# Performance work log

Hardware: AMD Instinct MI355X
Metric: run time of the kernel (lower is better)

The kernel has to match this reference:

```python
import jax, jax.numpy as jnp
import numpy as np

EPS = 1e-08


def conv(x, w, b, stride):
    y = jax.lax.conv_general_dilated(x, w, (stride, stride), 'VALID',
                                     dimension_numbers=('NCHW', 'OIHW', 'NCHW'))
    return y + b[None, :, None, None]


def cnn(x, p):
    x = jax.nn.relu(conv(x, p['c1w'], p['c1b'], 4))
    x = jax.nn.relu(conv(x, p['c2w'], p['c2b'], 2))
    x = jax.nn.relu(conv(x, p['c3w'], p['c3b'], 1))
    x = x.reshape(x.shape[0], -1)  # [B, 3136]
    return jax.nn.relu(x @ p['fcw'] + p['fcb'])  # [B, 256]


def mrn_distance(x, y):
    # x: [B,1,D], y: [1,B,D]
    d = x.shape[-1]
    max_component = jnp.max(jax.nn.relu(x[..., :d // 2] - y[..., :d // 2]), axis=-1)
    l2_component = jnp.sqrt(jnp.sum(jnp.square(x[..., d // 2:] - y[..., d // 2:]), axis=-1) + EPS)
    return max_component + l2_component


def setup_inputs() -> dict:
    key = jax.random.key(0)
    ks = jax.random.split(key, 20)
    B, C, H, W = 512, 4, 84, 84
    F, D = 256, 64
    flat = 7 * 7 * 64  # conv output for 84x84

    def w(k, shape, fan_in):
        return jax.random.normal(k, shape, jnp.float32) * (1.0 / np.sqrt(fan_in))

    return {
        'curr_obs': jax.random.uniform(ks[0], (B, C, H, W), jnp.float32),
        'next_obs': jax.random.uniform(ks[1], (B, C, H, W), jnp.float32),
        'c1w': w(ks[2], (32, C, 8, 8), C * 64), 'c1b': jnp.zeros((32,), jnp.float32),
        'c2w': w(ks[3], (64, 32, 4, 4), 32 * 16), 'c2b': jnp.zeros((64,), jnp.float32),
        'c3w': w(ks[4], (64, 64, 3, 3), 64 * 9), 'c3b': jnp.zeros((64,), jnp.float32),
        'fcw': w(ks[5], (flat, F), flat), 'fcb': jnp.zeros((F,), jnp.float32),
        'e1w': w(ks[6], (F, F), F), 'e1b': jnp.zeros((F,), jnp.float32),
        'e2w': w(ks[7], (F, D), F), 'e2b': jnp.zeros((D,), jnp.float32),
        'pw1': w(ks[8], (F, F), F), 'pb1': jnp.zeros((F,), jnp.float32),
        'pw2': w(ks[9], (F, 1), F), 'pb2': jnp.zeros((1,), jnp.float32),
    }


def reference(curr_obs, next_obs, c1w, c1b, c2w, c2b, c3w, c3b, fcw, fcb,
              e1w, e1b, e2w, e2b, pw1, pb1, pw2, pb2):
    p = dict(c1w=c1w, c1b=c1b, c2w=c2w, c2b=c2b, c3w=c3w, c3b=c3b, fcw=fcw, fcb=fcb)
    curr_f = cnn(curr_obs, p)
    next_f = cnn(next_obs, p)
    encode = lambda f: jax.nn.relu(f @ e1w + e1b) @ e2w + e2b
    phi_x = encode(curr_f)                                   # [B, D]
    phi_y = encode(next_f)                                   # [B, D]
    c_y = jax.nn.relu(next_f @ pw1 + pb1) @ pw2 + pb2        # [B, 1]

    # energy_fn == 'mrn_pot': potential bias minus pairwise MRN distance
    logits = c_y.T - mrn_distance(phi_x[:, None], phi_y[None, :])  # [B, B]

    B = logits.shape[0]
    # infonce: cross-entropy with labels arange(B) == -mean diag(log_softmax)
    logp = jax.nn.log_softmax(logits, axis=1)
    contrastive_loss = -jnp.mean(jnp.diagonal(logp))
    logsumexp_loss = jnp.mean(jax.nn.logsumexp(logits + 1e-06, axis=1) ** 2)
    total_loss = contrastive_loss + 0.1 * logsumexp_loss
    return total_loss
```

## Files before the change

kernel.cpp:

```cpp
#include <hip/hip_runtime.h>
#include <math.h>

typedef __attribute__((ext_vector_type(8))) short bf16x8;
typedef __attribute__((ext_vector_type(4))) float f32x4;

static __device__ __forceinline__ ushort f2bf(float x) {
    union { float f; unsigned u; } a; a.f = x;
    unsigned r = a.u + 0x7fff + ((a.u >> 16) & 1);
    return (ushort)(r >> 16);
}

__global__ __launch_bounds__(256) void repack_all_k(const float* __restrict__ c1w,
                                                    const float* __restrict__ c2w,
                                                    const float* __restrict__ c3w,
                                                    const float* __restrict__ fcw,
                                                    ushort* __restrict__ wp1,
                                                    ushort* __restrict__ wp2,
                                                    ushort* __restrict__ wp3,
                                                    ushort* __restrict__ wfc) {
    const int blk = blockIdx.x;
    if (blk < 32) {
        const int t = blk * 256 + threadIdx.x;
        const int j = t & 7, l = (t >> 3) & 63, kk = (t >> 9) & 7, ot = t >> 12;
        const int oc = ot * 16 + (l & 15);
        const int k  = kk * 32 + ((l >> 4) * 8) + j;
        wp1[t] = f2bf(c1w[oc * 256 + k]);
    } else if (blk < 160) {
        const int t = (blk - 32) * 256 + threadIdx.x;
        const int j = t & 7, l = (t >> 3) & 63, kk = (t >> 9) & 15, wv = t >> 13;
        const int oc = wv * 16 + (l & 15);
        const int k  = kk * 32 + ((l >> 4) * 8) + j;
        wp2[t] = f2bf(c2w[oc * 512 + k]);
    } else if (blk < 304) {
        const int t = (blk - 160) * 256 + threadIdx.x;
        const int j = t & 7, l = (t >> 3) & 63, kk = (t >> 9) & 1;
        const int ot = (t >> 10) & 3, kp = t >> 12;
        const int oc = ot * 16 + (l & 15);
        const int ic = kk * 32 + ((l >> 4) * 8) + j;
        wp3[t] = f2bf(c3w[(oc * 64 + ic) * 9 + kp]);
    } else {
        const int t = (blk - 304) * 256 + threadIdx.x;
        const int n = t / 3136, kp = t % 3136;
        const int pos = kp >> 6, oc = kp & 63;
        wfc[t] = f2bf(fcw[(oc * 49 + pos) * 256 + n]);
    }
}

__global__ __launch_bounds__(512, 4) void convs_k(const float* __restrict__ curr,
                                                  const float* __restrict__ nxt,
                                                  const ushort* __restrict__ wp1g,
                                                  const float* __restrict__ b1,
                                                  const ushort* __restrict__ wp2g,
                                                  const float* __restrict__ b2,
                                                  const ushort* __restrict__ wp3g,
                                                  const float* __restrict__ b3,
                                                  ushort* __restrict__ a3out) {
    __shared__ ushort stage[4 * 44 * 84];
    __shared__ ushort xt1[12800];
    const int tid = threadIdx.x;
    const int img = blockIdx.x;
    const float* xb = (img >= 512 ? nxt + (size_t)(img - 512) * 28224
                                  : curr + (size_t)img * 28224);

    const int w8 = tid >> 6;
    const int l = tid & 63, quad = l >> 4, col = l & 15;
    const bf16x8* wp1f = (const bf16x8*)wp1g;
    const bf16x8* wp2f = (const bf16x8*)wp2g;
    const bf16x8* wp3f = (const bf16x8*)wp3g;

    float bv1[2][4];
    #pragma unroll
    for (int ot = 0; ot < 2; ++ot)
        #pragma unroll
        for (int r = 0; r < 4; ++r) bv1[ot][r] = b1[ot * 16 + quad * 4 + r];

    for (int sup = 0; sup < 2; ++sup) {
        if (sup) __syncthreads();
        const int ih0 = sup * 40;
        for (int i = tid; i < 3696; i += 512) {
            const int row = i / 21, c4 = i % 21;
            const int ic = row / 44, rr = row % 44;
            const float4 v = *(const float4*)(xb + ic * 7056 + (ih0 + rr) * 84 + c4 * 4);
            ushort4 u; u.x = f2bf(v.x); u.y = f2bf(v.y); u.z = f2bf(v.z); u.w = f2bf(v.w);
            *(ushort4*)(stage + (ic * 44 + rr) * 84 + c4 * 4) = u;
        }
        __syncthreads();

        for (int t = w8; t < 13; t += 8) {
            const int lraw = t * 16 + col;
            const int lpos = lraw < 200 ? lraw : 199;
            const int ohl = lpos / 20, ow = lpos % 20;
            f32x4 acc0 = {0.f, 0.f, 0.f, 0.f}, acc1 = {0.f, 0.f, 0.f, 0.f};
            #pragma unroll
            for (int kk = 0; kk < 8; ++kk) {
                const bf16x8 a0 = wp1f[kk * 64 + l];
                const bf16x8 a1 = wp1f[(8 + kk) * 64 + l];
                const int ickh = kk * 4 + quad;
                const int ic = ickh >> 3, kh = ickh & 7;
                const int base = ic * 3696 + (ohl * 4 + kh) * 84 + ow * 4;
                union { uint2 u2[2]; bf16x8 v; } f;
                f.u2[0] = *(const uint2*)(stage + base);
                f.u2[1] = *(const uint2*)(stage + base + 4);
                acc0 = __builtin_amdgcn_mfma_f32_16x16x32_bf16(a0, f.v, acc0, 0, 0, 0);
                acc1 = __builtin_amdgcn_mfma_f32_16x16x32_bf16(a1, f.v, acc1, 0, 0, 0);
            }
            if (lraw < 200) {
                const int pos = sup * 200 + lraw;
                #pragma unroll
                for (int r = 0; r < 4; ++r) {
                    xt1[(quad * 4 + r) * 400 + pos]      = f2bf(fmaxf(acc0[r] + bv1[0][r], 0.f));
                    xt1[(16 + quad * 4 + r) * 400 + pos] = f2bf(fmaxf(acc1[r] + bv1[1][r], 0.f));
                }
            }
        }
    }
    __syncthreads();
    ushort* xt2 = stage;

    {
        const int oct = w8 & 3, half = w8 >> 2;
        int ohs[3], ows[3];
        #pragma unroll
        for (int tt = 0; tt < 3; ++tt) {
            int pos = (half * 3 + tt) * 16 + col; if (pos > 80) pos = 80;
            ohs[tt] = pos / 9; ows[tt] = pos % 9;
        }
        const int ic_off = quad >> 1;
        const int kh2    = (quad & 1) * 2;

        float bias_v[4];
        #pragma unroll
        for (int r2 = 0; r2 < 4; ++r2) bias_v[r2] = b2[oct * 16 + quad * 4 + r2];

        f32x4 acc[3];
        #pragma unroll
        for (int tt = 0; tt < 3; ++tt) acc[tt] = (f32x4){0.f, 0.f, 0.f, 0.f};

        for (int kk = 0; kk < 16; ++kk) {
            const bf16x8 a = wp2f[(oct * 16 + kk) * 64 + l];
            const int ic = kk * 2 + ic_off;
            #pragma unroll
            for (int tt = 0; tt < 3; ++tt) {
                const int base = ic * 400 + (ohs[tt] * 2 + kh2) * 20 + ows[tt] * 2;
                const unsigned* p0 = (const unsigned*)(xt1 + base);
                const unsigned* p1 = (const unsigned*)(xt1 + base + 20);
                union { unsigned u[4]; bf16x8 v; } f;
                f.u[0] = p0[0]; f.u[1] = p0[1];
                f.u[2] = p1[0]; f.u[3] = p1[1];
                acc[tt] = __builtin_amdgcn_mfma_f32_16x16x32_bf16(a, f.v, acc[tt], 0, 0, 0);
            }
        }
        __syncthreads();
        #pragma unroll
        for (int tt = 0; tt < 3; ++tt) {
            const int pos = (half * 3 + tt) * 16 + col;
            if (pos < 81) {
                ushort4 u;
                u.x = f2bf(fmaxf(acc[tt][0] + bias_v[0], 0.f));
                u.y = f2bf(fmaxf(acc[tt][1] + bias_v[1], 0.f));
                u.z = f2bf(fmaxf(acc[tt][2] + bias_v[2], 0.f));
                u.w = f2bf(fmaxf(acc[tt][3] + bias_v[3], 0.f));
                *(ushort4*)(xt2 + pos * 68 + oct * 16 + quad * 4) = u;
            }
        }
    }
    __syncthreads();

    {
        const int oct = w8 & 3, half = w8 >> 2;
        int ohs[2], ows[2];
        #pragma unroll
        for (int pt = 0; pt < 2; ++pt) {
            int pos = (half * 2 + pt) * 16 + col; if (pos > 48) pos = 48;
            ohs[pt] = pos / 7; ows[pt] = pos % 7;
        }
        float bv[4];
        #pragma unroll
        for (int r = 0; r < 4; ++r) bv[r] = b3[oct * 16 + quad * 4 + r];

        f32x4 acc[2];
        #pragma unroll
        for (int pt = 0; pt < 2; ++pt) acc[pt] = (f32x4){0.f, 0.f, 0.f, 0.f};

        #pragma unroll
        for (int kp = 0; kp < 9; ++kp) {
            const int kh = kp / 3, kw = kp % 3;
            #pragma unroll
            for (int kk = 0; kk < 2; ++kk) {
                const bf16x8 a = wp3f[((kp * 4 + oct) * 2 + kk) * 64 + l];
                #pragma unroll
                for (int pt = 0; pt < 2; ++pt) {
                    const int rpos = (ohs[pt] + kh) * 9 + (ows[pt] + kw);
                    const int base = rpos * 68 + kk * 32 + quad * 8;
                    union { uint2 u2[2]; bf16x8 v; } f;
                    f.u2[0] = *(const uint2*)(xt2 + base);
                    f.u2[1] = *(const uint2*)(xt2 + base + 4);
                    acc[pt] = __builtin_amdgcn_mfma_f32_16x16x32_bf16(a, f.v, acc[pt], 0, 0, 0);
                }
            }
        }
        #pragma unroll
        for (int pt = 0; pt < 2; ++pt) {
            const int pos = (half * 2 + pt) * 16 + col;
            if (pos < 49) {
                ushort4 u;
                u.x = f2bf(fmaxf(acc[pt][0] + bv[0], 0.f));
                u.y = f2bf(fmaxf(acc[pt][1] + bv[1], 0.f));
                u.z = f2bf(fmaxf(acc[pt][2] + bv[2], 0.f));
                u.w = f2bf(fmaxf(acc[pt][3] + bv[3], 0.f));
                *(ushort4*)(a3out + (size_t)img * 3136 + pos * 64 + oct * 16 + quad * 4) = u;
            }
        }
    }
}

__global__ __launch_bounds__(256) void fc_mfma_k(const ushort* __restrict__ a3,
                                                 const ushort* __restrict__ wfc,
                                                 const float* __restrict__ bias,
                                                 float* __restrict__ feat) {
    const int tid = threadIdx.x;
    const int gw = blockIdx.x * 4 + (tid >> 6);
    const int l = tid & 63, q = l >> 4, col = l & 15;
    const int mtile = gw >> 3, np = gw & 7;

    const ushort* arow = a3 + (size_t)(mtile * 16 + col) * 3136;
    const ushort* brow0 = wfc + (size_t)(np * 32 + col) * 3136;
    const ushort* brow1 = brow0 + (size_t)16 * 3136;

    f32x4 acc0 = {0.f, 0.f, 0.f, 0.f}, acc1 = {0.f, 0.f, 0.f, 0.f};
    #pragma unroll 2
    for (int kk = 0; kk < 98; ++kk) {
        const int ko = kk * 32 + q * 8;
        const bf16x8 av = *(const bf16x8*)(arow + ko);
        const bf16x8 b0 = *(const bf16x8*)(brow0 + ko);
        const bf16x8 b1 = *(const bf16x8*)(brow1 + ko);
        acc0 = __builtin_amdgcn_mfma_f32_16x16x32_bf16(av, b0, acc0, 0, 0, 0);
        acc1 = __builtin_amdgcn_mfma_f32_16x16x32_bf16(av, b1, acc1, 0, 0, 0);
    }

    #pragma unroll
    for (int r = 0; r < 4; ++r) {
        const int m = mtile * 16 + q * 4 + r;
        const int n0 = np * 32 + col, n1 = n0 + 16;
        feat[m * 256 + n0] = fmaxf(acc0[r] + bias[n0], 0.f);
        feat[m * 256 + n1] = fmaxf(acc1[r] + bias[n1], 0.f);
    }
}

__global__ __launch_bounds__(256) void heads_k(const float* __restrict__ feat,
                                               const float* __restrict__ e1w,
                                               const float* __restrict__ e1b,
                                               const float* __restrict__ e2w,
                                               const float* __restrict__ e2b,
                                               const float* __restrict__ pw1,
                                               const float* __restrict__ pb1,
                                               const float* __restrict__ pw2,
                                               const float* __restrict__ pb2,
                                               float* __restrict__ phi_x,
                                               float* __restrict__ phiYT,
                                               float* __restrict__ c_y,
                                               float* __restrict__ accbuf) {
    __shared__ float fc[2][256], fn[2][256];
    __shared__ float h1c[2][256], h1n[2][256], hp[2][256];
    const int tid = threadIdx.x;
    const int b0 = blockIdx.x * 2;

    if (blockIdx.x == 0 && tid < 4) accbuf[tid] = 0.f;

    for (int i = tid; i < 512; i += 256) {
        const int rr = i >> 8, c = i & 255;
        fc[rr][c] = feat[(b0 + rr) * 256 + c];
        fn[rr][c] = feat[131072 + (b0 + rr) * 256 + c];
    }
    __syncthreads();

    float ac0 = e1b[tid], ac1 = ac0;
    float an0 = ac0, an1 = ac0;
    float ap0 = pb1[tid], ap1 = ap0;
    for (int k = 0; k < 256; ++k) {
        const float we = e1w[k * 256 + tid];
        const float wpv = pw1[k * 256 + tid];
        ac0 += fc[0][k] * we;  ac1 += fc[1][k] * we;
        an0 += fn[0][k] * we;  an1 += fn[1][k] * we;
        ap0 += fn[0][k] * wpv; ap1 += fn[1][k] * wpv;
    }
    h1c[0][tid] = fmaxf(ac0, 0.f); h1c[1][tid] = fmaxf(ac1, 0.f);
    h1n[0][tid] = fmaxf(an0, 0.f); h1n[1][tid] = fmaxf(an1, 0.f);
    hp[0][tid]  = fmaxf(ap0, 0.f); hp[1][tid]  = fmaxf(ap1, 0.f);
    __syncthreads();

    const int wave = tid >> 6, lane = tid & 63;
    if (wave == 0) {
        #pragma unroll
        for (int rr = 0; rr < 2; ++rr) {
            float s = e2b[lane];
            for (int k = 0; k < 256; ++k) s += h1c[rr][k] * e2w[k * 64 + lane];
            phi_x[(b0 + rr) * 64 + lane] = s;
        }
    } else if (wave == 1) {
        #pragma unroll
        for (int rr = 0; rr < 2; ++rr) {
            float s = e2b[lane];
            for (int k = 0; k < 256; ++k) s += h1n[rr][k] * e2w[k * 64 + lane];
            phiYT[lane * 512 + b0 + rr] = s;
        }
    } else {
        const int rr = wave - 2;
        float s = 0.f;
        #pragma unroll
        for (int q2 = 0; q2 < 4; ++q2) s += hp[rr][lane * 4 + q2] * pw2[lane * 4 + q2];
        #pragma unroll
        for (int off = 32; off > 0; off >>= 1) s += __shfl_down(s, off);
        if (lane == 0) c_y[b0 + rr] = s + pb2[0];
    }
}

__global__ __launch_bounds__(256) void row_lse_loss_k(const float* __restrict__ phi_x,
                                                      const float* __restrict__ phiYT,
                                                      const float* __restrict__ c_y,
                                                      float* __restrict__ accbuf,
                                                      float* __restrict__ out) {
    const int i = blockIdx.x, tid = threadIdx.x;
    __shared__ float px[64];
    __shared__ float red[256];
    __shared__ float sdiag;
    if (tid < 64) px[tid] = phi_x[i * 64 + tid];
    __syncthreads();

    float lg[2];
    #pragma unroll
    for (int q = 0; q < 2; ++q) {
        const int j = tid + q * 256;
        float m = -1e30f;
        #pragma unroll 8
        for (int k = 0; k < 32; ++k) m = fmaxf(m, px[k] - phiYT[k * 512 + j]);
        const float maxc = fmaxf(m, 0.f);
        float s = 0.f;
        #pragma unroll 8
        for (int k = 32; k < 64; ++k) {
            const float d = px[k] - phiYT[k * 512 + j];
            s += d * d;
        }
        lg[q] = c_y[j] - (maxc + sqrtf(s + 1e-8f));
    }
    if ((i & 255) == tid) sdiag = lg[i >> 8];

    red[tid] = fmaxf(lg[0], lg[1]);
    __syncthreads();
    for (int s = 128; s > 0; s >>= 1) {
        if (tid < s) red[tid] = fmaxf(red[tid], red[tid + s]);
        __syncthreads();
    }
    const float m = red[0];
    __syncthreads();
    red[tid] = expf(lg[0] - m) + expf(lg[1] - m);
    __syncthreads();
    for (int s = 128; s > 0; s >>= 1) {
        if (tid < s) red[tid] += red[tid + s];
        __syncthreads();
    }

    if (tid == 0) {
        const float lse = m + logf(red[0]);
        const float l2 = lse + 1e-6f;
        atomicAdd(&accbuf[0], lse - sdiag);
        atomicAdd(&accbuf[1], l2 * l2);
        __threadfence();
        const unsigned old = atomicAdd((unsigned*)&accbuf[2], 1u);
        if (old == 511u) {
            __threadfence();
            const float s1 = atomicAdd(&accbuf[0], 0.f);
            const float s2 = atomicAdd(&accbuf[1], 0.f);
            out[0] = s1 / 512.f + 0.1f * (s2 / 512.f);
        }
    }
}

extern "C" void kernel_launch(void* const* d_in, const int* in_sizes, int n_in,
                              void* d_out, int out_size, void* d_ws, size_t ws_size,
                              hipStream_t stream) {
    const float* curr = (const float*)d_in[0];
    const float* nxt  = (const float*)d_in[1];
    const float* c1w  = (const float*)d_in[2];
    const float* c1b  = (const float*)d_in[3];
    const float* c2w  = (const float*)d_in[4];
    const float* c2b  = (const float*)d_in[5];
    const float* c3w  = (const float*)d_in[6];
    const float* c3b  = (const float*)d_in[7];
    const float* fcw  = (const float*)d_in[8];
    const float* fcb  = (const float*)d_in[9];
    const float* e1w  = (const float*)d_in[10];
    const float* e1b  = (const float*)d_in[11];
    const float* e2w  = (const float*)d_in[12];
    const float* e2b  = (const float*)d_in[13];
    const float* pw1  = (const float*)d_in[14];
    const float* pb1  = (const float*)d_in[15];
    const float* pw2  = (const float*)d_in[16];
    const float* pb2  = (const float*)d_in[17];

    ushort* a3  = (ushort*)d_ws;
    ushort* wp1 = a3 + 3211264;
    ushort* wp2 = wp1 + 8192;
    ushort* wp3 = wp2 + 32768;
    ushort* wfc = wp3 + 36864;
    float*  feat  = (float*)(wfc + 802816);
    float*  phi_x = feat + 262144;
    float*  phiYT = phi_x + 32768;
    float*  c_y   = phiYT + 32768;
    float*  acc   = c_y + 512;

    repack_all_k<<<3440, 256, 0, stream>>>(c1w, c2w, c3w, fcw, wp1, wp2, wp3, wfc);
    convs_k<<<1024, 512, 0, stream>>>(curr, nxt, wp1, c1b, wp2, c2b, wp3, c3b, a3);
    fc_mfma_k<<<128, 256, 0, stream>>>(a3, wfc, fcb, feat);
    heads_k<<<256, 256, 0, stream>>>(feat, e1w, e1b, e2w, e2b, pw1, pb1, pw2, pb2,
                                     phi_x, phiYT, c_y, acc);
    row_lse_loss_k<<<512, 256, 0, stream>>>(phi_x, phiYT, c_y, acc, (float*)d_out);
}
```

Baseline: 316.7 us.

## Halve conv LDS staging, pad xt1 stride, split-K the FC GEMM

```diff
diff --git a/kernel.cpp b/kernel.cpp
--- a/kernel.cpp
+++ b/kernel.cpp
@@ -9,6 +9,8 @@
     unsigned r = a.u + 0x7fff + ((a.u >> 16) & 1);
     return (ushort)(r >> 16);
 }
+
+#define XT1_P 404
 
 __global__ __launch_bounds__(256) void repack_all_k(const float* __restrict__ c1w,
                                                     const float* __restrict__ c2w,
@@ -40,13 +42,13 @@
         wp3[t] = f2bf(c3w[(oc * 64 + ic) * 9 + kp]);
     } else {
         const int t = (blk - 304) * 256 + threadIdx.x;
-        const int n = t / 3136, kp = t % 3136;
-        const int pos = kp >> 6, oc = kp & 63;
-        wfc[t] = f2bf(fcw[(oc * 49 + pos) * 256 + n]);
-    }
-}
-
-__global__ __launch_bounds__(512, 4) void convs_k(const float* __restrict__ curr,
+        const int k = t >> 8, n = t & 255;
+        const int oc = k / 49, pos = k % 49;
+        wfc[n * 3136 + pos * 64 + oc] = f2bf(fcw[t]);
+    }
+}
+
+__global__ __launch_bounds__(512, 8) void convs_k(const float* __restrict__ curr,
                                                   const float* __restrict__ nxt,
                                                   const ushort* __restrict__ wp1g,
                                                   const float* __restrict__ b1,
@@ -55,8 +57,8 @@
                                                   const ushort* __restrict__ wp3g,
                                                   const float* __restrict__ b3,
                                                   ushort* __restrict__ a3out) {
-    __shared__ ushort stage[4 * 44 * 84];
-    __shared__ ushort xt1[12800];
+    __shared__ ushort stage[2 * 44 * 84];
+    __shared__ ushort xt1[32 * XT1_P];
     const int tid = threadIdx.x;
     const int img = blockIdx.x;
     const float* xb = (img >= 512 ? nxt + (size_t)(img - 512) * 28224
@@ -75,41 +77,58 @@
         for (int r = 0; r < 4; ++r) bv1[ot][r] = b1[ot * 16 + quad * 4 + r];
 
     for (int sup = 0; sup < 2; ++sup) {
-        if (sup) __syncthreads();
+        f32x4 acc[2][2];
+        #pragma unroll
+        for (int ti = 0; ti < 2; ++ti)
+            #pragma unroll
+            for (int ot = 0; ot < 2; ++ot) acc[ti][ot] = (f32x4){0.f, 0.f, 0.f, 0.f};
+
         const int ih0 = sup * 40;
-        for (int i = tid; i < 3696; i += 512) {
-            const int row = i / 21, c4 = i % 21;
-            const int ic = row / 44, rr = row % 44;
-            const float4 v = *(const float4*)(xb + ic * 7056 + (ih0 + rr) * 84 + c4 * 4);
-            ushort4 u; u.x = f2bf(v.x); u.y = f2bf(v.y); u.z = f2bf(v.z); u.w = f2bf(v.w);
-            *(ushort4*)(stage + (ic * 44 + rr) * 84 + c4 * 4) = u;
-        }
-        __syncthreads();
-
-        for (int t = w8; t < 13; t += 8) {
+        for (int half = 0; half < 2; ++half) {
+            if (sup | half) __syncthreads();
+            for (int i = tid; i < 1848; i += 512) {
+                const int row = i / 21, c4 = i % 21;
+                const int icl = row / 44, rr = row % 44;
+                const float4 v = *(const float4*)(xb + (half * 2 + icl) * 7056 + (ih0 + rr) * 84 + c4 * 4);
+                ushort4 u; u.x = f2bf(v.x); u.y = f2bf(v.y); u.z = f2bf(v.z); u.w = f2bf(v.w);
+                *(ushort4*)(stage + (icl * 44 + rr) * 84 + c4 * 4) = u;
+            }
+            __syncthreads();
+
+            #pragma unroll
+            for (int ti = 0; ti < 2; ++ti) {
+                const int t = w8 + ti * 8;
+                if (t < 13) {
+                    const int lraw = t * 16 + col;
+                    const int lpos = lraw < 200 ? lraw : 199;
+                    const int ohl = lpos / 20, ow = lpos % 20;
+                    #pragma unroll
+                    for (int kk = 0; kk < 4; ++kk) {
+                        const int kkg = half * 4 + kk;
+                        const bf16x8 a0 = wp1f[kkg * 64 + l];
+                        const bf16x8 a1 = wp1f[(8 + kkg) * 64 + l];
+                        const int ickh = kkg * 4 + quad;
+                        const int icl = (ickh >> 3) & 1, kh = ickh & 7;
+                        const int base = icl * 3696 + (ohl * 4 + kh) * 84 + ow * 4;
+                        union { uint2 u2[2]; bf16x8 v; } f;
+                        f.u2[0] = *(const uint2*)(stage + base);
+                        f.u2[1] = *(const uint2*)(stage + base + 4);
+                        acc[ti][0] = __builtin_amdgcn_mfma_f32_16x16x32_bf16(a0, f.v, acc[ti][0], 0, 0, 0);
+                        acc[ti][1] = __builtin_amdgcn_mfma_f32_16x16x32_bf16(a1, f.v, acc[ti][1], 0, 0, 0);
+                    }
+                }
+            }
+        }
+        #pragma unroll
+        for (int ti = 0; ti < 2; ++ti) {
+            const int t = w8 + ti * 8;
             const int lraw = t * 16 + col;
-            const int lpos = lraw < 200 ? lraw : 199;
-            const int ohl = lpos / 20, ow = lpos % 20;
-            f32x4 acc0 = {0.f, 0.f, 0.f, 0.f}, acc1 = {0.f, 0.f, 0.f, 0.f};
-            #pragma unroll
-            for (int kk = 0; kk < 8; ++kk) {
-                const bf16x8 a0 = wp1f[kk * 64 + l];
-                const bf16x8 a1 = wp1f[(8 + kk) * 64 + l];
-                const int ickh = kk * 4 + quad;
-                const int ic = ickh >> 3, kh = ickh & 7;
-                const int base = ic * 3696 + (ohl * 4 + kh) * 84 + ow * 4;
-                union { uint2 u2[2]; bf16x8 v; } f;
-                f.u2[0] = *(const uint2*)(stage + base);
-                f.u2[1] = *(const uint2*)(stage + base + 4);
-                acc0 = __builtin_amdgcn_mfma_f32_16x16x32_bf16(a0, f.v, acc0, 0, 0, 0);
-                acc1 = __builtin_amdgcn_mfma_f32_16x16x32_bf16(a1, f.v, acc1, 0, 0, 0);
-            }
-            if (lraw < 200) {
+            if (t < 13 && lraw < 200) {
                 const int pos = sup * 200 + lraw;
                 #pragma unroll
                 for (int r = 0; r < 4; ++r) {
-                    xt1[(quad * 4 + r) * 400 + pos]      = f2bf(fmaxf(acc0[r] + bv1[0][r], 0.f));
-                    xt1[(16 + quad * 4 + r) * 400 + pos] = f2bf(fmaxf(acc1[r] + bv1[1][r], 0.f));
+                    xt1[(quad * 4 + r) * XT1_P + pos]      = f2bf(fmaxf(acc[ti][0][r] + bv1[0][r], 0.f));
+                    xt1[(16 + quad * 4 + r) * XT1_P + pos] = f2bf(fmaxf(acc[ti][1][r] + bv1[1][r], 0.f));
                 }
             }
         }
@@ -141,7 +160,7 @@
             const int ic = kk * 2 + ic_off;
             #pragma unroll
             for (int tt = 0; tt < 3; ++tt) {
-                const int base = ic * 400 + (ohs[tt] * 2 + kh2) * 20 + ows[tt] * 2;
+                const int base = ic * XT1_P + (ohs[tt] * 2 + kh2) * 20 + ows[tt] * 2;
                 const unsigned* p0 = (const unsigned*)(xt1 + base);
                 const unsigned* p1 = (const unsigned*)(xt1 + base + 20);
                 union { unsigned u[4]; bf16x8 v; } f;
@@ -218,32 +237,35 @@
                                                  const ushort* __restrict__ wfc,
                                                  const float* __restrict__ bias,
                                                  float* __restrict__ feat) {
+    __shared__ f32x4 red[2][64];
     const int tid = threadIdx.x;
-    const int gw = blockIdx.x * 4 + (tid >> 6);
-    const int l = tid & 63, q = l >> 4, col = l & 15;
-    const int mtile = gw >> 3, np = gw & 7;
-
-    const ushort* arow = a3 + (size_t)(mtile * 16 + col) * 3136;
-    const ushort* brow0 = wfc + (size_t)(np * 32 + col) * 3136;
-    const ushort* brow1 = brow0 + (size_t)16 * 3136;
-
-    f32x4 acc0 = {0.f, 0.f, 0.f, 0.f}, acc1 = {0.f, 0.f, 0.f, 0.f};
-    #pragma unroll 2
-    for (int kk = 0; kk < 98; ++kk) {
+    const int wid = tid >> 6, l = tid & 63, q = l >> 4, col = l & 15;
+    const int unit = blockIdx.x * 2 + (wid >> 1);
+    const int kh = wid & 1;
+    const int mtile = unit >> 4, nt = unit & 15;
+
+    const ushort* arow = a3 + (size_t)(mtile * 16 + col) * 3136 + kh * 1568;
+    const ushort* brow = wfc + (size_t)(nt * 16 + col) * 3136 + kh * 1568;
+
+    f32x4 acc = {0.f, 0.f, 0.f, 0.f};
+    #pragma unroll 7
+    for (int kk = 0; kk < 49; ++kk) {
         const int ko = kk * 32 + q * 8;
         const bf16x8 av = *(const bf16x8*)(arow + ko);
-        const bf16x8 b0 = *(const bf16x8*)(brow0 + ko);
-        const bf16x8 b1 = *(const bf16x8*)(brow1 + ko);
-        acc0 = __builtin_amdgcn_mfma_f32_16x16x32_bf16(av, b0, acc0, 0, 0, 0);
-        acc1 = __builtin_amdgcn_mfma_f32_16x16x32_bf16(av, b1, acc1, 0, 0, 0);
-    }
-
-    #pragma unroll
-    for (int r = 0; r < 4; ++r) {
-        const int m = mtile * 16 + q * 4 + r;
-        const int n0 = np * 32 + col, n1 = n0 + 16;
-        feat[m * 256 + n0] = fmaxf(acc0[r] + bias[n0], 0.f);
-        feat[m * 256 + n1] = fmaxf(acc1[r] + bias[n1], 0.f);
+        const bf16x8 bv = *(const bf16x8*)(brow + ko);
+        acc = __builtin_amdgcn_mfma_f32_16x16x32_bf16(av, bv, acc, 0, 0, 0);
+    }
+
+    if (kh == 1) red[wid >> 1][l] = acc;
+    __syncthreads();
+    if (kh == 0) {
+        const f32x4 other = red[wid >> 1][l];
+        #pragma unroll
+        for (int r = 0; r < 4; ++r) {
+            const int m = mtile * 16 + q * 4 + r;
+            const int n = nt * 16 + col;
+            feat[m * 256 + n] = fmaxf(acc[r] + other[r] + bias[n], 0.f);
+        }
     }
 }
 
@@ -411,7 +433,7 @@
 
     repack_all_k<<<3440, 256, 0, stream>>>(c1w, c2w, c3w, fcw, wp1, wp2, wp3, wfc);
     convs_k<<<1024, 512, 0, stream>>>(curr, nxt, wp1, c1b, wp2, c2b, wp3, c3b, a3);
-    fc_mfma_k<<<128, 256, 0, stream>>>(a3, wfc, fcb, feat);
+    fc_mfma_k<<<512, 256, 0, stream>>>(a3, wfc, fcb, feat);
     heads_k<<<256, 256, 0, stream>>>(feat, e1w, e1b, e2w, e2b, pw1, pb1, pw2, pb2,
                                      phi_x, phiYT, c_y, acc);
     row_lse_loss_k<<<512, 256, 0, stream>>>(phi_x, phiYT, c_y, acc, (float*)d_out);
```

Measured after the change: 302.1 us. 4.6% less time.
